# Performance work log

Measured on AMD Instinct MI355X. Metric: run time of the kernel, lower is better.

Reference implementation:

```python
import jax, jax.numpy as jnp
import numpy as np

B, S, D, H, V = 4, 1024, 2048, 16, 32000
LAYERS, DFF, HID, NSENT, NLAB = 2, 8192, 100, 3, 3
HD = D // H
LN2 = 0.6931471805599453


def _ln(x, g, b):
    m = jnp.mean(x, axis=-1, keepdims=True)
    v = jnp.mean((x - m) ** 2, axis=-1, keepdims=True)
    return (x - m) * jax.lax.rsqrt(v + 1e-5) * g + b


def setup_inputs():
    key = jax.random.key(0)
    ks = jax.random.split(key, 12)
    s = 0.02
    return dict(
        input_ids=jax.random.randint(ks[0], (B, S), 0, V),
        attention_mask=jnp.ones((B, S), dtype=jnp.int32),
        sentiment=jax.random.normal(ks[1], (B, NSENT), dtype=jnp.float32),
        perplexity=jax.random.uniform(ks[2], (B,), dtype=jnp.float32) + 1.0,
        emb=jax.random.normal(ks[3], (V, D), dtype=jnp.float32) * s,
        ln1_g=jnp.ones((LAYERS, D)), ln1_b=jnp.zeros((LAYERS, D)),
        qkv_w=jax.random.normal(ks[4], (LAYERS, D, 3 * D), dtype=jnp.float32) * s,
        wo_w=jax.random.normal(ks[5], (LAYERS, D, D), dtype=jnp.float32) * s,
        ln2_g=jnp.ones((LAYERS, D)), ln2_b=jnp.zeros((LAYERS, D)),
        w1=jax.random.normal(ks[6], (LAYERS, D, DFF), dtype=jnp.float32) * s,
        w2=jax.random.normal(ks[7], (LAYERS, DFF, D), dtype=jnp.float32) * s,
        lnf_g=jnp.ones((D,)), lnf_b=jnp.zeros((D,)),
        head_w=jax.random.normal(ks[8], (D, V), dtype=jnp.float32) * s,
        red_w=jax.random.normal(ks[9], (D, HID), dtype=jnp.float32) * s,
        red_b=jnp.zeros((HID,)),
        cls_w=jax.random.normal(ks[10], (HID + NSENT + 2, NLAB), dtype=jnp.float32) * s,
        cls_b=jnp.zeros((NLAB,)),
    )


def _lm(input_ids, attention_mask, emb, ln1_g, ln1_b, qkv_w, wo_w, ln2_g, ln2_b, w1, w2, lnf_g, lnf_b, head_w):
    x = emb[input_ids]  # [B,S,D]
    amask = attention_mask.astype(jnp.float32)
    causal = jnp.tril(jnp.ones((S, S), dtype=bool))
    bias = jnp.where(causal[None, None, :, :] & (amask[:, None, None, :] > 0), 0.0, -1e9)
    for l in range(LAYERS):
        h = _ln(x, ln1_g[l], ln1_b[l])
        qkv = h @ qkv_w[l]  # [B,S,3D]
        q, k, v = [t.reshape(B, S, H, HD) for t in jnp.split(qkv, 3, axis=-1)]
        scores = jnp.einsum('bqhd,bkhd->bhqk', q, k) / np.float32(np.sqrt(HD)) + bias
        attn = jax.nn.softmax(scores, axis=-1)
        o = jnp.einsum('bhqk,bkhd->bqhd', attn, v).reshape(B, S, D)
        x = x + o @ wo_w[l]
        h = _ln(x, ln2_g[l], ln2_b[l])
        x = x + jax.nn.gelu(h @ w1[l]) @ w2[l]
    h = _ln(x, lnf_g, lnf_b)
    logits = h @ head_w  # [B,S,V]
    return h, logits


def reference(input_ids, attention_mask, sentiment, perplexity, emb, ln1_g, ln1_b, qkv_w, wo_w, ln2_g, ln2_b, w1, w2, lnf_g, lnf_b, head_w, red_w, red_b, cls_w, cls_b):
    h, logits = _lm(input_ids, attention_mask, emb, ln1_g, ln1_b, qkv_w, wo_w,
                    ln2_g, ln2_b, w1, w2, lnf_g, lnf_b, head_w)
    amask = attention_mask.astype(jnp.float32)
    pooled = jnp.mean(h, axis=1)  # mean over seq -> [B,D]
    # probs = softmax(logits).detach(); gather own token prob; -log2(p)
    lg = jax.lax.stop_gradient(logits)
    logZ = jax.scipy.special.logsumexp(lg, axis=-1)  # [B,S]
    tok_logit = jnp.take_along_axis(lg, input_ids[..., None], axis=-1)[..., 0]
    subword_surp = -(tok_logit - logZ) / LN2 * amask
    mean_surprisal = subword_surp.sum(axis=1) / amask.sum(axis=1)  # [B]
    r = jax.nn.leaky_relu(pooled @ red_w + red_b)  # torch intent: LeakyReLU after reducer
    feats = jnp.concatenate([r, sentiment, perplexity[:, None], mean_surprisal[:, None]], axis=1)
    return feats @ cls_w + cls_b  # [B, NLAB]
```

## Files before the change

### kernel.cpp

```cpp
#include <hip/hip_runtime.h>

typedef unsigned short u16;
typedef __bf16 bf16x8 __attribute__((ext_vector_type(8)));
typedef float f32x4 __attribute__((ext_vector_type(4)));

__device__ __forceinline__ u16 f2bf(float f){
  unsigned u = __float_as_uint(f);
  unsigned r = u + 0x7FFFu + ((u >> 16) & 1u);
  return (u16)(r >> 16);
}
__device__ __forceinline__ float bf2f(u16 v){ return __uint_as_float(((unsigned)v) << 16); }

__device__ __forceinline__ void gload16(const void* g, void* l){
  __builtin_amdgcn_global_load_lds(
      (const __attribute__((address_space(1))) unsigned int*)g,
      (__attribute__((address_space(3))) unsigned int*)l, 16, 0, 0);
}

__global__ __launch_bounds__(256) void transp_k(const float* __restrict__ in, u16* __restrict__ out, int K, int N)
{
  __shared__ float tl[64][65];
  const int n0 = blockIdx.x * 64, k0 = blockIdx.y * 64;
  const int t = threadIdx.x;
  const int r = t >> 4, c4 = t & 15;
#pragma unroll
  for (int i = 0; i < 4; ++i){
    float4 v = *(const float4*)(in + (size_t)(k0 + r + i*16) * N + n0 + c4*4);
    tl[r + i*16][c4*4 + 0] = v.x; tl[r + i*16][c4*4 + 1] = v.y;
    tl[r + i*16][c4*4 + 2] = v.z; tl[r + i*16][c4*4 + 3] = v.w;
  }
  __syncthreads();
#pragma unroll
  for (int i = 0; i < 4; ++i){
    const int n = r + i*16;
    ushort4 o;
    o.x = f2bf(tl[c4*4 + 0][n]); o.y = f2bf(tl[c4*4 + 1][n]);
    o.z = f2bf(tl[c4*4 + 2][n]); o.w = f2bf(tl[c4*4 + 3][n]);
    *(ushort4*)(out + (size_t)(n0 + n) * K + k0 + c4*4) = o;
  }
}

__global__ __launch_bounds__(256) void embed_k(const int* __restrict__ ids, const float* __restrict__ emb, float* __restrict__ x)
{
  const int row = blockIdx.x;
  const int c = blockIdx.y * 256 + threadIdx.x;
  x[(size_t)row * 2048 + c] = emb[(size_t)ids[row] * 2048 + c];
}

__global__ __launch_bounds__(256) void ln_k(const float* __restrict__ x, const float* __restrict__ gw,
                                            const float* __restrict__ bw, u16* __restrict__ o)
{
  const int row = blockIdx.x, t = threadIdx.x;
  const int lane = t & 63, wid = t >> 6;
  const float4* xr = (const float4*)(x + (size_t)row * 2048);
  float4 v1 = xr[t], v2 = xr[t + 256];
  float s1 = v1.x + v1.y + v1.z + v1.w + v2.x + v2.y + v2.z + v2.w;
  float s2 = v1.x*v1.x + v1.y*v1.y + v1.z*v1.z + v1.w*v1.w
           + v2.x*v2.x + v2.y*v2.y + v2.z*v2.z + v2.w*v2.w;
#pragma unroll
  for (int off = 32; off >= 1; off >>= 1){ s1 += __shfl_down(s1, off); s2 += __shfl_down(s2, off); }
  __shared__ float rb[2][4];
  __shared__ float mv[2];
  if (lane == 0){ rb[0][wid] = s1; rb[1][wid] = s2; }
  __syncthreads();
  if (t == 0){
    float a = rb[0][0] + rb[0][1] + rb[0][2] + rb[0][3];
    float q = rb[1][0] + rb[1][1] + rb[1][2] + rb[1][3];
    float mean = a * (1.f/2048.f);
    float var  = q * (1.f/2048.f) - mean*mean;
    mv[0] = mean; mv[1] = rsqrtf(var + 1e-5f);
  }
  __syncthreads();
  const float mean = mv[0], rstd = mv[1];
  const float4* g4 = (const float4*)gw;
  const float4* b4 = (const float4*)bw;
  float4 ga = g4[t], ba = b4[t], gb = g4[t + 256], bb2 = b4[t + 256];
  ushort4 o1, o2;
  o1.x = f2bf((v1.x - mean)*rstd*ga.x + ba.x);
  o1.y = f2bf((v1.y - mean)*rstd*ga.y + ba.y);
  o1.z = f2bf((v1.z - mean)*rstd*ga.z + ba.z);
  o1.w = f2bf((v1.w - mean)*rstd*ga.w + ba.w);
  o2.x = f2bf((v2.x - mean)*rstd*gb.x + bb2.x);
  o2.y = f2bf((v2.y - mean)*rstd*gb.y + bb2.y);
  o2.z = f2bf((v2.z - mean)*rstd*gb.z + bb2.z);
  o2.w = f2bf((v2.w - mean)*rstd*gb.w + bb2.w);
  ((ushort4*)(o + (size_t)row * 2048))[t] = o1;
  ((ushort4*)(o + (size_t)row * 2048))[t + 256] = o2;
}

enum { M_QKV = 0, M_RES = 1, M_GELU = 2, M_LSE = 3 };

template<int MODE, int BM>
__global__ __launch_bounds__(512, 2) void gemm2_k(
    const u16* __restrict__ A, const u16* __restrict__ BT,
    int N, int K, int MB,
    u16* __restrict__ outb, float* __restrict__ outf,
    float* __restrict__ partial, float* __restrict__ tokl,
    const int* __restrict__ ids, u16* __restrict__ vtout)
{
  constexpr int BK  = 32;
  constexpr int ASZ = BM * BK;
  constexpr int BSZ = 256 * BK;
  constexpr int BUF = ASZ + BSZ;
  constexpr int NFR = BM / 32;
  __shared__ u16 lds[3 * BUF];

  const int tid  = threadIdx.x;
  const int wv   = tid >> 6, lane = tid & 63;
  const int wr   = wv >> 2,  wc   = wv & 3;
  const int lg   = lane >> 4, lr  = lane & 15;

  const int nwg = gridDim.x;
  const int bid = blockIdx.x;
  const int swz = ((nwg & 7) == 0) ? ((bid & 7) * (nwg >> 3) + (bid >> 3)) : bid;
  const int bm = swz % MB, bn = swz / MB;
  const int m0 = bm * BM, n0 = bn * 256;

  const int ll = lane >> 3;
  const int cc = lane & 7;
  const int lc = cc ^ ll;
  const int gr = (ll << 1) + (lc >> 2);
  const int gk = (lc & 3) << 3;

  const u16* gA = A  + (size_t)m0 * K + gk;
  const u16* gB = BT + (size_t)n0 * K + gk;

  f32x4 acc[NFR][4];
#pragma unroll
  for (int i = 0; i < NFR; ++i)
#pragma unroll
    for (int j = 0; j < 4; ++j)
#pragma unroll
      for (int r = 0; r < 4; ++r) acc[i][j][r] = 0.f;

  const int nt = K >> 5;

  auto STAGE = [&](int bi, int kt){
    char* bA = (char*)lds + (size_t)bi * BUF * 2;
    char* bB = bA + ASZ * 2;
    const size_t ko = (size_t)kt * 32;
    if constexpr (BM == 256){
      gload16(gA + (size_t)((wv    ) * 16 + gr) * K + ko, bA + (wv    ) * 1024);
      gload16(gA + (size_t)((wv + 8) * 16 + gr) * K + ko, bA + (wv + 8) * 1024);
    } else {
      gload16(gA + (size_t)(wv * 16 + gr) * K + ko, bA + wv * 1024);
    }
    gload16(gB + (size_t)((wv    ) * 16 + gr) * K + ko, bB + (wv    ) * 1024);
    gload16(gB + (size_t)((wv + 8) * 16 + gr) * K + ko, bB + (wv + 8) * 1024);
  };

  STAGE(0, 0);
  STAGE(1, 1);

  for (int t = 0; t < nt; ++t){
    if (t + 1 < nt){
      if constexpr (BM == 256) asm volatile("s_waitcnt vmcnt(4) lgkmcnt(0)" ::: "memory");
      else                     asm volatile("s_waitcnt vmcnt(3) lgkmcnt(0)" ::: "memory");
    } else {
      asm volatile("s_waitcnt vmcnt(0) lgkmcnt(0)" ::: "memory");
    }
    __builtin_amdgcn_s_barrier();
    if (t + 2 < nt) STAGE((t + 2) % 3, t + 2);

    const char* bA = (const char*)lds + (size_t)(t % 3) * BUF * 2;
    const char* bB = bA + ASZ * 2;
    bf16x8 af[NFR], bq[4];
#pragma unroll
    for (int i = 0; i < NFR; ++i){
      const int ra = wr * (BM / 2) + i * 16 + lr;
      const int p = ra >> 1;
      const int slot = (((ra & 1) << 2) | lg) ^ (p & 7);
      af[i] = *(const bf16x8*)(bA + p * 128 + slot * 16);
    }
#pragma unroll
    for (int j = 0; j < 4; ++j){
      const int rb = wc * 64 + j * 16 + lr;
      const int p = rb >> 1;
      const int slot = (((rb & 1) << 2) | lg) ^ (p & 7);
      bq[j] = *(const bf16x8*)(bB + p * 128 + slot * 16);
    }
    __builtin_amdgcn_s_setprio(1);
#pragma unroll
    for (int i = 0; i < NFR; ++i)
#pragma unroll
      for (int j = 0; j < 4; ++j)
        acc[i][j] = __builtin_amdgcn_mfma_f32_16x16x32_bf16(af[i], bq[j], acc[i][j], 0, 0, 0);
    __builtin_amdgcn_s_setprio(0);
  }

#pragma unroll
  for (int i = 0; i < NFR; ++i){
#pragma unroll
    for (int r = 0; r < 4; ++r){
      const int row = m0 + wr * (BM / 2) + i * 16 + lg * 4 + r;
#pragma unroll
      for (int j = 0; j < 4; ++j){
        const int col = n0 + wc * 64 + j * 16 + lr;
        const float v = acc[i][j][r];
        if constexpr (MODE == M_RES){
          float* pp = outf + (size_t)row * N + col;
          *pp += v;
        } else if constexpr (MODE == M_GELU){
          float u = 0.7978845608028654f * (v + 0.044715f * v * v * v);
          u = fminf(fmaxf(u, -15.f), 15.f);
          const float ex = __expf(2.f * u);
          const float th = (ex - 1.f) / (ex + 1.f);
          outb[(size_t)row * N + col] = f2bf(0.5f * v * (1.f + th));
        }
      }
    }
  }
}

template<int MODE>
__global__ __launch_bounds__(512, 2) void gemm6_k(
    const u16* __restrict__ A, const u16* __restrict__ BT,
    int N, int K, int MB,
    u16* __restrict__ outb, float* __restrict__ outf,
    float* __restrict__ partial, float* __restrict__ tokl,
    const int* __restrict__ ids, u16* __restrict__ vtout)
{
  __shared__ u16 lds[65536];

  const int tid  = threadIdx.x;
  const int wv   = tid >> 6, lane = tid & 63;
  const int wr   = wv >> 2,  wc   = wv & 3;
  const int lg   = lane >> 4, lr  = lane & 15;

  const int nwg = gridDim.x;
  const int bid = blockIdx.x;
  const int swz = ((nwg & 7) == 0) ? ((bid & 7) * (nwg >> 3) + (bid >> 3)) : bid;
  const int bm = swz % MB, bn = swz / MB;
  const int m0 = bm * 256, n0 = bn * 256;

  const int ll = lane >> 3;
  const int cc = lane & 7;
  const int lc = cc ^ ll;
  const int gr = (ll << 1) + (lc >> 2);
  const int gk = (lc & 3) << 3;

  const u16* gA = A  + (size_t)m0 * K + gk;
  const u16* gB = BT + (size_t)n0 * K + gk;

  f32x4 acc[8][4];
#pragma unroll
  for (int i = 0; i < 8; ++i)
#pragma unroll
    for (int j = 0; j < 4; ++j)
#pragma unroll
      for (int r = 0; r < 4; ++r) acc[i][j][r] = 0.f;

  const int nt = K >> 6;

  auto RB = [&](int tt, int kh, int bsel) -> char* {
    return (char*)lds + (((tt & 1) << 16) | (kh << 15) | (bsel << 14));
  };
  auto STG = [&](const u16* gsrc, int tt, int kh, int bsel){
    char* dst = RB(tt, kh, bsel);
    const size_t ko = (size_t)tt * 64 + kh * 32;
    gload16(gsrc + (size_t)((wv    ) * 16 + gr) * K + ko, dst + (wv    ) * 1024);
    gload16(gsrc + (size_t)((wv + 8) * 16 + gr) * K + ko, dst + (wv + 8) * 1024);
  };
  auto FRG = [&](int tt, int kh, int bsel, int row) -> bf16x8 {
    const int p = row >> 1;
    const int slot = (((row & 1) << 2) | lg) ^ (p & 7);
    return *(const bf16x8*)(RB(tt, kh, bsel) + p * 128 + slot * 16);
  };

  STG(gA, 0, 0, 0); STG(gB, 0, 0, 1);
  STG(gA, 0, 1, 0); STG(gB, 0, 1, 1);
  STG(gA, 1, 0, 0); STG(gB, 1, 0, 1);
  asm volatile("s_waitcnt vmcnt(4)" ::: "memory");
  __builtin_amdgcn_s_barrier();

  for (int u = 0; u < nt; ++u){
    bf16x8 bq[4], aa[4];
#pragma unroll
    for (int j = 0; j < 4; ++j) bq[j] = FRG(u, 0, 1, wc * 64 + j * 16 + lr);
#pragma unroll
    for (int i = 0; i < 4; ++i) aa[i] = FRG(u, 0, 0, wr * 128 + i * 16 + lr);
    if (u + 1 < nt) STG(gA, u + 1, 1, 0);
    __builtin_amdgcn_s_barrier();
    asm volatile("s_waitcnt lgkmcnt(0)" ::: "memory");
    __builtin_amdgcn_s_setprio(1);
#pragma unroll
    for (int i = 0; i < 4; ++i)
#pragma unroll
      for (int j = 0; j < 4; ++j)
        acc[i][j] = __builtin_amdgcn_mfma_f32_16x16x32_bf16(aa[i], bq[j], acc[i][j], 0, 0, 0);
    __builtin_amdgcn_s_setprio(0);
    __builtin_amdgcn_s_barrier();

    bf16x8 ab[4];
#pragma unroll
    for (int i = 0; i < 4; ++i) ab[i] = FRG(u, 0, 0, wr * 128 + (4 + i) * 16 + lr);
    if (u + 1 < nt) STG(gB, u + 1, 1, 1);
    __builtin_amdgcn_s_barrier();
    asm volatile("s_waitcnt lgkmcnt(0)" ::: "memory");
    __builtin_amdgcn_s_setprio(1);
#pragma unroll
    for (int i = 0; i < 4; ++i)
#pragma unroll
      for (int j = 0; j < 4; ++j)
        acc[4 + i][j] = __builtin_amdgcn_mfma_f32_16x16x32_bf16(ab[i], bq[j], acc[4 + i][j], 0, 0, 0);
    __builtin_amdgcn_s_setprio(0);
    __builtin_amdgcn_s_barrier();

    bf16x8 bq2[4], ac[4];
#pragma unroll
    for (int j = 0; j < 4; ++j) bq2[j] = FRG(u, 1, 1, wc * 64 + j * 16 + lr);
#pragma unroll
    for (int i = 0; i < 4; ++i) ac[i] = FRG(u, 1, 0, wr * 128 + i * 16 + lr);
    if (u + 2 < nt) STG(gA, u + 2, 0, 0);
    __builtin_amdgcn_s_barrier();
    asm volatile("s_waitcnt lgkmcnt(0)" ::: "memory");
    __builtin_amdgcn_s_setprio(1);
#pragma unroll
    for (int i = 0; i < 4; ++i)
#pragma unroll
      for (int j = 0; j < 4; ++j)
        acc[i][j] = __builtin_amdgcn_mfma_f32_16x16x32_bf16(ac[i], bq2[j], acc[i][j], 0, 0, 0);
    __builtin_amdgcn_s_setprio(0);
    __builtin_amdgcn_s_barrier();

    bf16x8 ad[4];
#pragma unroll
    for (int i = 0; i < 4; ++i) ad[i] = FRG(u, 1, 0, wr * 128 + (4 + i) * 16 + lr);
    if (u + 2 < nt) STG(gB, u + 2, 0, 1);
    if (u + 2 < nt)      asm volatile("s_waitcnt vmcnt(4)" ::: "memory");
    else if (u + 1 < nt) asm volatile("s_waitcnt vmcnt(0)" ::: "memory");
    __builtin_amdgcn_s_barrier();
    asm volatile("s_waitcnt lgkmcnt(0)" ::: "memory");
    __builtin_amdgcn_s_setprio(1);
#pragma unroll
    for (int i = 0; i < 4; ++i)
#pragma unroll
      for (int j = 0; j < 4; ++j)
        acc[4 + i][j] = __builtin_amdgcn_mfma_f32_16x16x32_bf16(ad[i], bq2[j], acc[4 + i][j], 0, 0, 0);
    __builtin_amdgcn_s_setprio(0);
    __builtin_amdgcn_s_barrier();
  }

#pragma unroll
  for (int i = 0; i < 8; ++i){
    if constexpr (MODE == M_LSE){
#pragma unroll
      for (int r = 0; r < 4; ++r){
        const int row = m0 + wr * 128 + i * 16 + lg * 4 + r;
        const int id = ids[row];
        float esum = 0.f;
#pragma unroll
        for (int j = 0; j < 4; ++j){
          const int col = n0 + wc * 64 + j * 16 + lr;
          const float v = acc[i][j][r];
          if (col == id) tokl[row] = v;
          esum += __expf(v);
        }
#pragma unroll
        for (int off = 8; off >= 1; off >>= 1) esum += __shfl_xor(esum, off);
        if (lr == 0) partial[(size_t)row * 500 + bn * 4 + wc] = esum;
      }
    } else if constexpr (MODE == M_QKV){
#pragma unroll
      for (int j = 0; j < 4; ++j){
        const int colb = n0 + wc * 64 + j * 16;
        if (colb < 4096){
#pragma unroll
          for (int r = 0; r < 4; ++r){
            const int row = m0 + wr * 128 + i * 16 + lg * 4 + r;
            outb[(size_t)row * 6144 + colb + lr] = f2bf(acc[i][j][r]);
          }
        } else {
          const int srow = m0 + wr * 128 + i * 16 + lg * 4;
          const int b = srow >> 10, s = srow & 1023;
          int dd = colb + lr - 4096;
          const int hh = dd >> 7; dd &= 127;
          ushort4 o;
          o.x = f2bf(acc[i][j][0]); o.y = f2bf(acc[i][j][1]);
          o.z = f2bf(acc[i][j][2]); o.w = f2bf(acc[i][j][3]);
          *(ushort4*)(vtout + ((size_t)(b * 16 + hh) * 128 + dd) * 1024 + s) = o;
        }
      }
    } else {
#pragma unroll
      for (int r = 0; r < 4; ++r){
        const int row = m0 + wr * 128 + i * 16 + lg * 4 + r;
#pragma unroll
        for (int j = 0; j < 4; ++j){
          const int col = n0 + wc * 64 + j * 16 + lr;
          const float v = acc[i][j][r];
          if constexpr (MODE == M_RES){
            float* pp = outf + (size_t)row * N + col;
            *pp += v;
          } else {
            float u2 = 0.7978845608028654f * (v + 0.044715f * v * v * v);
            u2 = fminf(fmaxf(u2, -15.f), 15.f);
            const float ex = __expf(2.f * u2);
            const float th = (ex - 1.f) / (ex + 1.f);
            outb[(size_t)row * N + col] = f2bf(0.5f * v * (1.f + th));
          }
        }
      }
    }
  }
}

__global__ __launch_bounds__(64) void attn_k(const u16* __restrict__ qkv, const u16* __restrict__ vT, u16* __restrict__ o16)
{
  __shared__ u16 P[16 * 40];
  const int bid = blockIdx.x;
  const int qt = bid & 63, bh = bid >> 6;
  const int h = bh & 15, b = bh >> 4;
  const int lane = threadIdx.x, lg = lane >> 4, lr = lane & 15;
  const int q0 = qt << 4;
  const u16* qrow  = qkv + (size_t)(b * 1024 + q0 + lr) * 6144 + h * 128;
  const u16* krow  = qkv + (size_t)(b * 1024 + lr) * 6144 + 2048 + h * 128;
  const u16* vbase = vT + (size_t)(b * 16 + h) * 128 * 1024;

  bf16x8 qf[4];
#pragma unroll
  for (int c = 0; c < 4; ++c) qf[c] = *(const bf16x8*)(qrow + c * 32 + lg * 8);

  float m[4], l[4];
  f32x4 oacc[8];
#pragma unroll
  for (int r = 0; r < 4; ++r){ m[r] = -1e30f; l[r] = 0.f; }
#pragma unroll
  for (int f = 0; f < 8; ++f)
#pragma unroll
    for (int r = 0; r < 4; ++r) oacc[f][r] = 0.f;

  const float scale = 0.08838834764831845f;
  const int nk2 = (qt >> 1) + 1;
  for (int k2 = 0; k2 < nk2; ++k2){
    float e[2][4];
    float rmax[4];
#pragma unroll
    for (int r = 0; r < 4; ++r) rmax[r] = -1e30f;
#pragma unroll
    for (int hh = 0; hh < 2; ++hh){
      const int kt = k2 * 2 + hh;
      if (kt <= qt){
        f32x4 s;
#pragma unroll
        for (int r = 0; r < 4; ++r) s[r] = 0.f;
#pragma unroll
        for (int c = 0; c < 4; ++c){
          bf16x8 kf = *(const bf16x8*)(krow + (size_t)(kt * 16) * 6144 + c * 32 + lg * 8);
          s = __builtin_amdgcn_mfma_f32_16x16x32_bf16(qf[c], kf, s, 0, 0, 0);
        }
#pragma unroll
        for (int r = 0; r < 4; ++r){
          float sv = s[r] * scale;
          if (kt * 16 + lr > q0 + lg * 4 + r) sv = -1e30f;
          e[hh][r] = sv;
          rmax[r] = fmaxf(rmax[r], sv);
        }
      } else {
#pragma unroll
        for (int r = 0; r < 4; ++r) e[hh][r] = -1e30f;
      }
    }
#pragma unroll
    for (int off = 8; off >= 1; off >>= 1)
#pragma unroll
      for (int r = 0; r < 4; ++r) rmax[r] = fmaxf(rmax[r], __shfl_xor(rmax[r], off));
    float corr[4], rsum[4];
#pragma unroll
    for (int r = 0; r < 4; ++r){
      const float mn = fmaxf(m[r], rmax[r]);
      corr[r] = __expf(m[r] - mn);
      m[r] = mn;
      const float e0 = __expf(e[0][r] - mn);
      const float e1 = __expf(e[1][r] - mn);
      e[0][r] = e0; e[1][r] = e1;
      rsum[r] = e0 + e1;
    }
#pragma unroll
    for (int off = 8; off >= 1; off >>= 1)
#pragma unroll
      for (int r = 0; r < 4; ++r) rsum[r] += __shfl_xor(rsum[r], off);
#pragma unroll
    for (int r = 0; r < 4; ++r) l[r] = l[r] * corr[r] + rsum[r];
#pragma unroll
    for (int hh = 0; hh < 2; ++hh)
#pragma unroll
      for (int r = 0; r < 4; ++r)
        P[(lg * 4 + r) * 40 + hh * 16 + lr] = f2bf(e[hh][r]);
#pragma unroll
    for (int f = 0; f < 8; ++f)
#pragma unroll
      for (int r = 0; r < 4; ++r) oacc[f][r] = oacc[f][r] * corr[r];
    __syncthreads();
    const bf16x8 pa = *(const bf16x8*)((const u16*)P + lr * 40 + lg * 8);
#pragma unroll
    for (int f = 0; f < 8; ++f){
      bf16x8 vb = *(const bf16x8*)(vbase + (size_t)(f * 16 + lr) * 1024 + k2 * 32 + lg * 8);
      oacc[f] = __builtin_amdgcn_mfma_f32_16x16x32_bf16(pa, vb, oacc[f], 0, 0, 0);
    }
    __syncthreads();
  }
  u16* orow = o16 + (size_t)(b * 1024 + q0 + lg * 4) * 2048 + h * 128;
#pragma unroll
  for (int r = 0; r < 4; ++r){
    const float linv = 1.0f / l[r];
#pragma unroll
    for (int f = 0; f < 8; ++f)
      orow[(size_t)r * 2048 + f * 16 + lr] = f2bf(oacc[f][r] * linv);
  }
}

__global__ __launch_bounds__(256) void lse_k(const float* __restrict__ partial, const float* __restrict__ tokl,
                                             const int* __restrict__ amask, float* __restrict__ surp)
{
  const int row = blockIdx.x, t = threadIdx.x, lane = t & 63, wid = t >> 6;
  float s = 0.f;
  if (t < 250) s = partial[(size_t)row * 500 + t] + partial[(size_t)row * 500 + t + 250];
#pragma unroll
  for (int off = 32; off >= 1; off >>= 1) s += __shfl_down(s, off);
  __shared__ float rb[4];
  if (lane == 0) rb[wid] = s;
  __syncthreads();
  if (t == 0){
    const float tot = rb[0] + rb[1] + rb[2] + rb[3];
    surp[row] = (logf(tot) - tokl[row]) * 1.4426950408889634f * (float)amask[row];
  }
}

__global__ __launch_bounds__(256) void pool_k(const u16* __restrict__ h16, float* __restrict__ pooled)
{
  const int d = blockIdx.x * 256 + threadIdx.x;
  const int b = blockIdx.y;
  const u16* p = h16 + (size_t)b * 1024 * 2048 + d;
  float a0 = 0.f, a1 = 0.f, a2 = 0.f, a3 = 0.f;
  for (int s = 0; s < 1024; s += 4){
    a0 += bf2f(p[(size_t)(s + 0) * 2048]);
    a1 += bf2f(p[(size_t)(s + 1) * 2048]);
    a2 += bf2f(p[(size_t)(s + 2) * 2048]);
    a3 += bf2f(p[(size_t)(s + 3) * 2048]);
  }
  pooled[b * 2048 + d] = (a0 + a1 + a2 + a3) * (1.f / 1024.f);
}

__global__ __launch_bounds__(256) void cls_k(const float* __restrict__ pooled, const float* __restrict__ surp,
                                             const int* __restrict__ amask, const float* __restrict__ sent,
                                             const float* __restrict__ ppl, const float* __restrict__ redw,
                                             const float* __restrict__ redb, const float* __restrict__ clsw,
                                             const float* __restrict__ clsb, float* __restrict__ out)
{
  const int b = blockIdx.x, t = threadIdx.x;
  const int lane = t & 63, wid = t >> 6;
  __shared__ float pl[2048];
  __shared__ float feats[112];
  __shared__ float rbuf[2][4];
#pragma unroll
  for (int i = 0; i < 8; ++i) pl[t + i * 256] = pooled[b * 2048 + t + i * 256];
  float ssum = 0.f, msum = 0.f;
#pragma unroll
  for (int i = 0; i < 4; ++i){
    const int s = t + i * 256;
    ssum += surp[b * 1024 + s];
    msum += (float)amask[b * 1024 + s];
  }
#pragma unroll
  for (int off = 32; off >= 1; off >>= 1){ ssum += __shfl_down(ssum, off); msum += __shfl_down(msum, off); }
  if (lane == 0){ rbuf[0][wid] = ssum; rbuf[1][wid] = msum; }
  __syncthreads();
  if (t == 0){
    float a = 0.f, c = 0.f;
    for (int i = 0; i < 4; ++i){ a += rbuf[0][i]; c += rbuf[1][i]; }
    feats[104] = a / c;
  }
  if (t >= 100 && t < 103) feats[t] = sent[b * 3 + (t - 100)];
  if (t == 103) feats[103] = ppl[b];
  if (t < 100){
    float a = redb[t];
    for (int d = 0; d < 2048; ++d) a += pl[d] * redw[d * 100 + t];
    feats[t] = (a > 0.f) ? a : 0.01f * a;
  }
  __syncthreads();
  if (t < 3){
    float a = clsb[t];
    for (int i = 0; i < 105; ++i) a += feats[i] * clsw[i * 3 + t];
    out[b * 3 + t] = a;
  }
}

extern "C" void kernel_launch(void* const* d_in, const int* in_sizes, int n_in,
                              void* d_out, int out_size, void* d_ws, size_t ws_size,
                              hipStream_t stream)
{
  (void)in_sizes; (void)n_in; (void)out_size; (void)ws_size;
  const int*   ids   = (const int*)d_in[0];
  const int*   amask = (const int*)d_in[1];
  const float* sent  = (const float*)d_in[2];
  const float* ppl   = (const float*)d_in[3];
  const float* emb   = (const float*)d_in[4];
  const float* ln1g  = (const float*)d_in[5];
  const float* ln1b  = (const float*)d_in[6];
  const float* qkvw  = (const float*)d_in[7];
  const float* wow   = (const float*)d_in[8];
  const float* ln2g  = (const float*)d_in[9];
  const float* ln2b  = (const float*)d_in[10];
  const float* w1    = (const float*)d_in[11];
  const float* w2    = (const float*)d_in[12];
  const float* lnfg  = (const float*)d_in[13];
  const float* lnfb  = (const float*)d_in[14];
  const float* headw = (const float*)d_in[15];
  const float* redw  = (const float*)d_in[16];
  const float* redb  = (const float*)d_in[17];
  const float* clsw  = (const float*)d_in[18];
  const float* clsb  = (const float*)d_in[19];
  float* out = (float*)d_out;

  char* p = (char*)d_ws;
  u16* wqkvT = (u16*)p; p += (size_t)2 * 6144 * 2048 * 2;
  u16* woT   = (u16*)p; p += (size_t)2 * 2048 * 2048 * 2;
  u16* w1T   = (u16*)p; p += (size_t)2 * 8192 * 2048 * 2;
  u16* w2T   = (u16*)p; p += (size_t)2 * 2048 * 8192 * 2;
  u16* whT   = (u16*)p; p += (size_t)32000 * 2048 * 2;
  float* xbuf = (float*)p; p += (size_t)4096 * 2048 * 4;
  u16* h16   = (u16*)p; p += (size_t)4096 * 2048 * 2;
  u16* qkv16 = (u16*)p;
  u16* vT16  = (u16*)(p + (size_t)4096 * 6144 * 2);
  u16* ffn16 = (u16*)p;
  p += (size_t)4096 * 6144 * 2 + (size_t)4096 * 2048 * 2;
  u16* o16   = (u16*)p; p += (size_t)4096 * 2048 * 2;
  float* partial = (float*)p; p += (size_t)4096 * 500 * 4;
  float* tokl = (float*)p; p += (size_t)4096 * 4;
  float* surp = (float*)p; p += (size_t)4096 * 4;
  float* pooled = (float*)p; p += (size_t)4 * 2048 * 4;

  for (int l = 0; l < 2; ++l){
    transp_k<<<dim3(6144/64, 2048/64), 256, 0, stream>>>(qkvw + (size_t)l*2048*6144, wqkvT + (size_t)l*6144*2048, 2048, 6144);
    transp_k<<<dim3(2048/64, 2048/64), 256, 0, stream>>>(wow  + (size_t)l*2048*2048, woT   + (size_t)l*2048*2048, 2048, 2048);
    transp_k<<<dim3(8192/64, 2048/64), 256, 0, stream>>>(w1   + (size_t)l*2048*8192, w1T   + (size_t)l*8192*2048, 2048, 8192);
    transp_k<<<dim3(2048/64, 8192/64), 256, 0, stream>>>(w2   + (size_t)l*8192*2048, w2T   + (size_t)l*2048*8192, 8192, 2048);
  }
  transp_k<<<dim3(32000/64, 2048/64), 256, 0, stream>>>(headw, whT, 2048, 32000);

  embed_k<<<dim3(4096, 8), 256, 0, stream>>>(ids, emb, xbuf);

  for (int l = 0; l < 2; ++l){
    ln_k<<<4096, 256, 0, stream>>>(xbuf, ln1g + l*2048, ln1b + l*2048, h16);
    gemm6_k<M_QKV><<<16*24, 512, 0, stream>>>(h16, wqkvT + (size_t)l*6144*2048, 6144, 2048, 16,
                                              qkv16, nullptr, nullptr, nullptr, nullptr, vT16);
    attn_k<<<4096, 64, 0, stream>>>(qkv16, vT16, o16);
    gemm2_k<M_RES,128><<<32*8, 512, 0, stream>>>(o16, woT + (size_t)l*2048*2048, 2048, 2048, 32,
                                                 nullptr, xbuf, nullptr, nullptr, nullptr, nullptr);
    ln_k<<<4096, 256, 0, stream>>>(xbuf, ln2g + l*2048, ln2b + l*2048, h16);
    gemm6_k<M_GELU><<<16*32, 512, 0, stream>>>(h16, w1T + (size_t)l*8192*2048, 8192, 2048, 16,
                                               ffn16, nullptr, nullptr, nullptr, nullptr, nullptr);
    gemm2_k<M_RES,128><<<32*8, 512, 0, stream>>>(ffn16, w2T + (size_t)l*2048*8192, 2048, 8192, 32,
                                                 nullptr, xbuf, nullptr, nullptr, nullptr, nullptr);
  }
  ln_k<<<4096, 256, 0, stream>>>(xbuf, lnfg, lnfb, h16);
  gemm6_k<M_LSE><<<16*125, 512, 0, stream>>>(h16, whT, 32000, 2048, 16,
                                             nullptr, nullptr, partial, tokl, ids, nullptr);
  lse_k<<<4096, 256, 0, stream>>>(partial, tokl, amask, surp);
  pool_k<<<dim3(8, 4), 256, 0, stream>>>(h16, pooled);
  cls_k<<<4, 256, 0, stream>>>(pooled, surp, amask, sent, ppl, redw, redb, clsw, clsb, out);
}
```

Baseline: 2.340 ms.

## Run LM-head GEMM in FP8 with scaled weights and fused LSE epilogue

Quantizes the transposed head weights (scaled by 16) and the final layer-norm activations to FP8 e4m3, and adds a new FP8 MFMA GEMM kernel that computes the logsumexp partials and token logits for the 32000-wide vocabulary projection. This targets the largest GEMM, aiming to halve operand bandwidth and use the higher FP8 MFMA throughput. The final layer norm now also writes an FP8 copy of its output. The risk is accuracy loss in the logits and surprisal from e4m3 quantization, and the new kernel uses a simpler double-buffered pipeline than the tuned bf16 kernel.

```diff
diff --git a/kernel.cpp b/kernel.cpp
--- a/kernel.cpp
+++ b/kernel.cpp
@@ -1,6 +1,7 @@
 #include <hip/hip_runtime.h>
 
 typedef unsigned short u16;
+typedef unsigned char u8;
 typedef __bf16 bf16x8 __attribute__((ext_vector_type(8)));
 typedef float f32x4 __attribute__((ext_vector_type(4)));
 
@@ -10,6 +11,27 @@
   return (u16)(r >> 16);
 }
 __device__ __forceinline__ float bf2f(u16 v){ return __uint_as_float(((unsigned)v) << 16); }
+
+__device__ __forceinline__ u8 f2fp8(float f){
+  unsigned u = __float_as_uint(f);
+  u8 s = (u >> 24) & 0x80;
+  float a = __uint_as_float(u & 0x7FFFFFFF);
+  if (!(a < 464.f)) return s | 0x7E;
+  unsigned eu = u & 0x7F800000u;
+  unsigned cb = eu + (20u << 23);
+  const unsigned cmin = 141u << 23;
+  float c = __uint_as_float(cb > cmin ? cb : cmin);
+  float q = (a + c) - c;
+  if (q > 448.f) return s | 0x7E;
+  if (q == 0.f) return s;
+  unsigned uq = __float_as_uint(q);
+  int eq = (int)(uq >> 23) - 127;
+  if (eq < -6){
+    int mq = (int)(q * 512.f);
+    return s | (u8)mq;
+  }
+  return s | (u8)(((eq + 7) << 3) | ((uq >> 20) & 7));
+}
 
 __device__ __forceinline__ void gload16(const void* g, void* l){
   __builtin_amdgcn_global_load_lds(
@@ -40,6 +62,29 @@
   }
 }
 
+__global__ __launch_bounds__(256) void transp8_k(const float* __restrict__ in, u8* __restrict__ out, int K, int N)
+{
+  __shared__ float tl[64][65];
+  const int n0 = blockIdx.x * 64, k0 = blockIdx.y * 64;
+  const int t = threadIdx.x;
+  const int r = t >> 4, c4 = t & 15;
+#pragma unroll
+  for (int i = 0; i < 4; ++i){
+    float4 v = *(const float4*)(in + (size_t)(k0 + r + i*16) * N + n0 + c4*4);
+    tl[r + i*16][c4*4 + 0] = v.x; tl[r + i*16][c4*4 + 1] = v.y;
+    tl[r + i*16][c4*4 + 2] = v.z; tl[r + i*16][c4*4 + 3] = v.w;
+  }
+  __syncthreads();
+#pragma unroll
+  for (int i = 0; i < 4; ++i){
+    const int n = r + i*16;
+    uchar4 o;
+    o.x = f2fp8(tl[c4*4 + 0][n] * 16.f); o.y = f2fp8(tl[c4*4 + 1][n] * 16.f);
+    o.z = f2fp8(tl[c4*4 + 2][n] * 16.f); o.w = f2fp8(tl[c4*4 + 3][n] * 16.f);
+    *(uchar4*)(out + (size_t)(n0 + n) * K + k0 + c4*4) = o;
+  }
+}
+
 __global__ __launch_bounds__(256) void embed_k(const int* __restrict__ ids, const float* __restrict__ emb, float* __restrict__ x)
 {
   const int row = blockIdx.x;
@@ -47,8 +92,9 @@
   x[(size_t)row * 2048 + c] = emb[(size_t)ids[row] * 2048 + c];
 }
 
+template<bool FP8>
 __global__ __launch_bounds__(256) void ln_k(const float* __restrict__ x, const float* __restrict__ gw,
-                                            const float* __restrict__ bw, u16* __restrict__ o)
+                                            const float* __restrict__ bw, u16* __restrict__ o, u8* __restrict__ o8)
 {
   const int row = blockIdx.x, t = threadIdx.x;
   const int lane = t & 63, wid = t >> 6;
@@ -75,17 +121,26 @@
   const float4* g4 = (const float4*)gw;
   const float4* b4 = (const float4*)bw;
   float4 ga = g4[t], ba = b4[t], gb = g4[t + 256], bb2 = b4[t + 256];
+  float n1x = (v1.x - mean)*rstd*ga.x + ba.x;
+  float n1y = (v1.y - mean)*rstd*ga.y + ba.y;
+  float n1z = (v1.z - mean)*rstd*ga.z + ba.z;
+  float n1w = (v1.w - mean)*rstd*ga.w + ba.w;
+  float n2x = (v2.x - mean)*rstd*gb.x + bb2.x;
+  float n2y = (v2.y - mean)*rstd*gb.y + bb2.y;
+  float n2z = (v2.z - mean)*rstd*gb.z + bb2.z;
+  float n2w = (v2.w - mean)*rstd*gb.w + bb2.w;
   ushort4 o1, o2;
-  o1.x = f2bf((v1.x - mean)*rstd*ga.x + ba.x);
-  o1.y = f2bf((v1.y - mean)*rstd*ga.y + ba.y);
-  o1.z = f2bf((v1.z - mean)*rstd*ga.z + ba.z);
-  o1.w = f2bf((v1.w - mean)*rstd*ga.w + ba.w);
-  o2.x = f2bf((v2.x - mean)*rstd*gb.x + bb2.x);
-  o2.y = f2bf((v2.y - mean)*rstd*gb.y + bb2.y);
-  o2.z = f2bf((v2.z - mean)*rstd*gb.z + bb2.z);
-  o2.w = f2bf((v2.w - mean)*rstd*gb.w + bb2.w);
+  o1.x = f2bf(n1x); o1.y = f2bf(n1y); o1.z = f2bf(n1z); o1.w = f2bf(n1w);
+  o2.x = f2bf(n2x); o2.y = f2bf(n2y); o2.z = f2bf(n2z); o2.w = f2bf(n2w);
   ((ushort4*)(o + (size_t)row * 2048))[t] = o1;
   ((ushort4*)(o + (size_t)row * 2048))[t + 256] = o2;
+  if constexpr (FP8){
+    uchar4 q1, q2;
+    q1.x = f2fp8(n1x); q1.y = f2fp8(n1y); q1.z = f2fp8(n1z); q1.w = f2fp8(n1w);
+    q2.x = f2fp8(n2x); q2.y = f2fp8(n2y); q2.z = f2fp8(n2z); q2.w = f2fp8(n2w);
+    *(uchar4*)(o8 + (size_t)row * 2048 + t * 4) = q1;
+    *(uchar4*)(o8 + (size_t)row * 2048 + 1024 + t * 4) = q2;
+  }
 }
 
 enum { M_QKV = 0, M_RES = 1, M_GELU = 2, M_LSE = 3 };
@@ -343,24 +398,7 @@
 
 #pragma unroll
   for (int i = 0; i < 8; ++i){
-    if constexpr (MODE == M_LSE){
-#pragma unroll
-      for (int r = 0; r < 4; ++r){
-        const int row = m0 + wr * 128 + i * 16 + lg * 4 + r;
-        const int id = ids[row];
-        float esum = 0.f;
-#pragma unroll
-        for (int j = 0; j < 4; ++j){
-          const int col = n0 + wc * 64 + j * 16 + lr;
-          const float v = acc[i][j][r];
-          if (col == id) tokl[row] = v;
-          esum += __expf(v);
-        }
-#pragma unroll
-        for (int off = 8; off >= 1; off >>= 1) esum += __shfl_xor(esum, off);
-        if (lr == 0) partial[(size_t)row * 500 + bn * 4 + wc] = esum;
-      }
-    } else if constexpr (MODE == M_QKV){
+    if constexpr (MODE == M_QKV){
 #pragma unroll
       for (int j = 0; j < 4; ++j){
         const int colb = n0 + wc * 64 + j * 16;
@@ -401,6 +439,105 @@
           }
         }
       }
+    }
+  }
+}
+
+__global__ __launch_bounds__(512, 2) void gemm8_k(
+    const u8* __restrict__ A8, const u8* __restrict__ B8,
+    int N, int K, int MB,
+    float* __restrict__ partial, float* __restrict__ tokl,
+    const int* __restrict__ ids)
+{
+  __shared__ u8 lds8[2 * 16384];
+
+  const int tid  = threadIdx.x;
+  const int wv   = tid >> 6, lane = tid & 63;
+  const int wr   = wv >> 2,  wc   = wv & 3;
+  const int lg   = lane >> 4, lr  = lane & 15;
+
+  const int nwg = gridDim.x;
+  const int bid = blockIdx.x;
+  const int swz = ((nwg & 7) == 0) ? ((bid & 7) * (nwg >> 3) + (bid >> 3)) : bid;
+  const int bm = swz % MB, bn = swz / MB;
+  const int m0 = bm * 256, n0 = bn * 256;
+
+  const int sll = lane >> 3;
+  const int sq  = (lane & 7) ^ (sll & 3);
+  const int srow = sll * 4 + (sq >> 1);
+  const int skb  = (sq & 1) << 4;
+
+  const u8* gA = A8 + (size_t)(m0 + wv * 32 + srow) * K + skb;
+  const u8* gB = B8 + (size_t)(n0 + wv * 32 + srow) * K + skb;
+
+  f32x4 acc[8][4];
+#pragma unroll
+  for (int i = 0; i < 8; ++i)
+#pragma unroll
+    for (int j = 0; j < 4; ++j)
+#pragma unroll
+      for (int r = 0; r < 4; ++r) acc[i][j][r] = 0.f;
+
+  const int nt = K >> 5;
+
+  auto STAGE = [&](int bi, int kt){
+    u8* base = lds8 + bi * 16384;
+    gload16(gA + (size_t)kt * 32, base + wv * 1024);
+    gload16(gB + (size_t)kt * 32, base + 8192 + wv * 1024);
+  };
+
+  auto FR8 = [&](const u8* base, int r) -> long {
+    const int p = r >> 2;
+    const int gsw = (((r & 3) << 2) | lg) ^ ((p & 3) << 1);
+    return *(const long*)(base + p * 128 + gsw * 8);
+  };
+
+  STAGE(0, 0);
+  STAGE(1, 1);
+
+  for (int t = 0; t < nt; ++t){
+    if (t + 1 < nt) asm volatile("s_waitcnt vmcnt(2)" ::: "memory");
+    else            asm volatile("s_waitcnt vmcnt(0)" ::: "memory");
+    __builtin_amdgcn_s_barrier();
+
+    const u8* bA = lds8 + (t & 1) * 16384;
+    const u8* bB = bA + 8192;
+    long af[8], bq[4];
+#pragma unroll
+    for (int i = 0; i < 8; ++i) af[i] = FR8(bA, wr * 128 + i * 16 + lr);
+#pragma unroll
+    for (int j = 0; j < 4; ++j) bq[j] = FR8(bB, wc * 64 + j * 16 + lr);
+    asm volatile("s_waitcnt lgkmcnt(0)" ::: "memory");
+    __builtin_amdgcn_s_barrier();
+
+    if (t + 2 < nt) STAGE(t & 1, t + 2);
+
+    __builtin_amdgcn_s_setprio(1);
+#pragma unroll
+    for (int i = 0; i < 8; ++i)
+#pragma unroll
+      for (int j = 0; j < 4; ++j)
+        acc[i][j] = __builtin_amdgcn_mfma_f32_16x16x32_fp8_fp8(af[i], bq[j], acc[i][j], 0, 0, 0);
+    __builtin_amdgcn_s_setprio(0);
+  }
+
+#pragma unroll
+  for (int i = 0; i < 8; ++i){
+#pragma unroll
+    for (int r = 0; r < 4; ++r){
+      const int row = m0 + wr * 128 + i * 16 + lg * 4 + r;
+      const int id = ids[row];
+      float esum = 0.f;
+#pragma unroll
+      for (int j = 0; j < 4; ++j){
+        const int col = n0 + wc * 64 + j * 16 + lr;
+        const float v = acc[i][j][r] * 0.0625f;
+        if (col == id) tokl[row] = v;
+        esum += __expf(v);
+      }
+#pragma unroll
+      for (int off = 8; off >= 1; off >>= 1) esum += __shfl_xor(esum, off);
+      if (lr == 0) partial[(size_t)row * 500 + bn * 4 + wc] = esum;
     }
   }
 }
@@ -618,9 +755,10 @@
   u16* woT   = (u16*)p; p += (size_t)2 * 2048 * 2048 * 2;
   u16* w1T   = (u16*)p; p += (size_t)2 * 8192 * 2048 * 2;
   u16* w2T   = (u16*)p; p += (size_t)2 * 2048 * 8192 * 2;
-  u16* whT   = (u16*)p; p += (size_t)32000 * 2048 * 2;
+  u8*  wh8   = (u8*)p;  p += (size_t)32000 * 2048;
   float* xbuf = (float*)p; p += (size_t)4096 * 2048 * 4;
   u16* h16   = (u16*)p; p += (size_t)4096 * 2048 * 2;
+  u8*  h8    = (u8*)p;  p += (size_t)4096 * 2048;
   u16* qkv16 = (u16*)p;
   u16* vT16  = (u16*)(p + (size_t)4096 * 6144 * 2);
   u16* ffn16 = (u16*)p;
@@ -637,26 +775,25 @@
     transp_k<<<dim3(8192/64, 2048/64), 256, 0, stream>>>(w1   + (size_t)l*2048*8192, w1T   + (size_t)l*8192*2048, 2048, 8192);
     transp_k<<<dim3(2048/64, 8192/64), 256, 0, stream>>>(w2   + (size_t)l*8192*2048, w2T   + (size_t)l*2048*8192, 8192, 2048);
   }
-  transp_k<<<dim3(32000/64, 2048/64), 256, 0, stream>>>(headw, whT, 2048, 32000);
+  transp8_k<<<dim3(32000/64, 2048/64), 256, 0, stream>>>(headw, wh8, 2048, 32000);
 
   embed_k<<<dim3(4096, 8), 256, 0, stream>>>(ids, emb, xbuf);
 
   for (int l = 0; l < 2; ++l){
-    ln_k<<<4096, 256, 0, stream>>>(xbuf, ln1g + l*2048, ln1b + l*2048, h16);
+    ln_k<false><<<4096, 256, 0, stream>>>(xbuf, ln1g + l*2048, ln1b + l*2048, h16, nullptr);
     gemm6_k<M_QKV><<<16*24, 512, 0, stream>>>(h16, wqkvT + (size_t)l*6144*2048, 6144, 2048, 16,
                                               qkv16, nullptr, nullptr, nullptr, nullptr, vT16);
     attn_k<<<4096, 64, 0, stream>>>(qkv16, vT16, o16);
     gemm2_k<M_RES,128><<<32*8, 512, 0, stream>>>(o16, woT + (size_t)l*2048*2048, 2048, 2048, 32,
                                                  nullptr, xbuf, nullptr, nullptr, nullptr, nullptr);
-    ln_k<<<4096, 256, 0, stream>>>(xbuf, ln2g + l*2048, ln2b + l*2048, h16);
+    ln_k<false><<<4096, 256, 0, stream>>>(xbuf, ln2g + l*2048, ln2b + l*2048, h16, nullptr);
     gemm6_k<M_GELU><<<16*32, 512, 0, stream>>>(h16, w1T + (size_t)l*8192*2048, 8192, 2048, 16,
                                                ffn16, nullptr, nullptr, nullptr, nullptr, nullptr);
     gemm2_k<M_RES,128><<<32*8, 512, 0, stream>>>(ffn16, w2T + (size_t)l*2048*8192, 2048, 8192, 32,
                                                  nullptr, xbuf, nullptr, nullptr, nullptr, nullptr);
   }
-  ln_k<<<4096, 256, 0, stream>>>(xbuf, lnfg, lnfb, h16);
-  gemm6_k<M_LSE><<<16*125, 512, 0, stream>>>(h16, whT, 32000, 2048, 16,
-                                             nullptr, nullptr, partial, tokl, ids, nullptr);
+  ln_k<true><<<4096, 256, 0, stream>>>(xbuf, lnfg, lnfb, h16, h8);
+  gemm8_k<<<16*125, 512, 0, stream>>>(h8, wh8, 32000, 2048, 16, partial, tokl, ids);
   lse_k<<<4096, 256, 0, stream>>>(partial, tokl, amask, surp);
   pool_k<<<dim3(8, 4), 256, 0, stream>>>(h16, pooled);
   cls_k<<<4, 256, 0, stream>>>(pooled, surp, amask, sent, ppl, redw, redb, clsw, clsb, out);
```

Measured after the change: 2.363 ms. About the same (+1.0%).
